# Kernel tuning notes

Measured on AMD Instinct MI355X. Metric: run time of the kernel, lower is better.

Reference implementation:

```python
import jax, jax.numpy as jnp
import numpy as np

DIM = 1024
N_HEADS = 16
N_KV_HEADS = 4
HEAD_DIM = 64
BATCH = 1
SEQ = 4096
ROPE_BASE = 1000.0


def _rope_tables(seq_len, head_dim, base):
    theta = 1.0 / base ** (jnp.arange(0, head_dim, 2, dtype=jnp.float32) / head_dim)
    freqs = jnp.outer(jnp.arange(seq_len, dtype=jnp.float32), theta)  # [S, hd/2]
    return jnp.cos(freqs), jnp.sin(freqs)


def _apply_rope(x, cos, sin):
    # x: [B, S, H, hd]; cos/sin: [S, hd/2] -> broadcast [1, S, 1, hd/2]
    c = cos[None, :, None, :]
    s = sin[None, :, None, :]
    x1, x2 = x[..., ::2], x[..., 1::2]
    even = x1 * c - x2 * s
    odd = x1 * s + x2 * c
    return jnp.stack([even, odd], axis=-1).reshape(x.shape)


def setup_inputs() -> dict:
    key = jax.random.key(0)
    kx, kq, kk, kv, ko = jax.random.split(key, 5)
    x = jax.random.normal(kx, (BATCH, SEQ, DIM), dtype=jnp.float32)
    # causal mask (1 = attend, 0 = masked)
    mask = jnp.tril(jnp.ones((SEQ, SEQ), dtype=jnp.int32))[None, None, :, :]
    scale = DIM ** -0.5
    Wq = jax.random.normal(kq, (DIM, N_HEADS * HEAD_DIM), dtype=jnp.float32) * scale
    Wk = jax.random.normal(kk, (DIM, N_KV_HEADS * HEAD_DIM), dtype=jnp.float32) * scale
    Wv = jax.random.normal(kv, (DIM, N_KV_HEADS * HEAD_DIM), dtype=jnp.float32) * scale
    Wo = jax.random.normal(ko, (N_HEADS * HEAD_DIM, DIM), dtype=jnp.float32) * scale
    return {"x": x, "mask": mask, "Wq": Wq, "Wk": Wk, "Wv": Wv, "Wo": Wo}


def reference(x, mask, Wq, Wk, Wv, Wo):
    batch, seq_len, _ = x.shape
    q = (x @ Wq).reshape(batch, seq_len, N_HEADS, HEAD_DIM)
    k = (x @ Wk).reshape(batch, seq_len, N_KV_HEADS, HEAD_DIM)
    v = (x @ Wv).reshape(batch, seq_len, N_KV_HEADS, HEAD_DIM)
    cos, sin = _rope_tables(seq_len, HEAD_DIM, ROPE_BASE)
    q = _apply_rope(q, cos, sin)
    k = _apply_rope(k, cos, sin)
    rep = N_HEADS // N_KV_HEADS
    k = jnp.repeat(k, rep, axis=2)  # [B, S, H, hd]
    v = jnp.repeat(v, rep, axis=2)
    q = q.transpose(0, 2, 1, 3)  # [B, H, S, hd]
    k = k.transpose(0, 2, 1, 3)
    v = v.transpose(0, 2, 1, 3)
    scale = HEAD_DIM ** -0.5
    scores = jnp.einsum('bhqd,bhkd->bhqk', q, k) * scale  # [B, H, S, S]
    scores = jnp.where(mask == 0, -jnp.inf, scores)
    attn = jax.nn.softmax(scores, axis=-1)
    out = jnp.einsum('bhqk,bhkd->bhqd', attn, v)
    out = out.transpose(0, 2, 1, 3).reshape(batch, seq_len, N_HEADS * HEAD_DIM)
    return out @ Wo
```

## Files before the change

### kernel.cpp

```cpp
#include <hip/hip_runtime.h>
#include <hip/hip_bf16.h>

typedef __attribute__((ext_vector_type(8))) short short8;
typedef __attribute__((ext_vector_type(4))) float f32x4;
typedef unsigned short u16;
typedef unsigned int u32;

#define SEQ 4096

__device__ __forceinline__ u16 f2bf(float f) {
  return __builtin_bit_cast(u16, __float2bfloat16(f));
}

#if __has_builtin(__builtin_amdgcn_exp2f)
#define EXP2(x) __builtin_amdgcn_exp2f(x)
#else
#define EXP2(x) exp2f(x)
#endif

__device__ __forceinline__ u32 pk2(float a, float b) {
  u32 ua = __builtin_bit_cast(u32, a) + 0x8000u;
  u32 ub = __builtin_bit_cast(u32, b) + 0x8000u;
  return __builtin_amdgcn_perm(ub, ua, 0x07060302);
}

__device__ __forceinline__ u32 pk2t(float a, float b) {
  return __builtin_amdgcn_perm(__builtin_bit_cast(u32, b),
                               __builtin_bit_cast(u32, a), 0x07060302);
}

typedef __attribute__((address_space(1))) u32 gas_u32;
typedef __attribute__((address_space(3))) u32 las_u32;
__device__ __forceinline__ void gload16(const u16* g, const u16* l) {
  __builtin_amdgcn_global_load_lds((gas_u32*)(unsigned long long)(const void*)g,
                                   (las_u32*)(u32)(unsigned long long)(const void*)l,
                                   16, 0, 0);
}

#define VM_DRAIN() asm volatile("s_waitcnt vmcnt(0)" ::: "memory")

__global__ __launch_bounds__(256) void k_prep(const float* __restrict__ x,
                                              u16* __restrict__ xb,
                                              float* __restrict__ cosT,
                                              float* __restrict__ sinT) {
  int bid = blockIdx.x;
  if (bid < 4096) {
    int i = bid * 256 + threadIdx.x;
    float4 v = ((const float4*)x)[i];
    u32 lo = (u32)f2bf(v.x) | ((u32)f2bf(v.y) << 16);
    u32 hi = (u32)f2bf(v.z) | ((u32)f2bf(v.w) << 16);
    uint2 o; o.x = lo; o.y = hi;
    ((uint2*)xb)[i] = o;
  } else {
    int tid = (bid - 4096) * 256 + threadIdx.x;
    int pos = tid >> 5, j = tid & 31;
    float theta = exp2f(-0.311430758895f * (float)j);
    float a = (float)pos * theta;
    float s, c;
    sincosf(a, &s, &c);
    cosT[tid] = c;
    sinT[tid] = s;
  }
}

__global__ __launch_bounds__(256) void k_tconvW(const float* __restrict__ Wq,
                                                const float* __restrict__ Wk,
                                                const float* __restrict__ Wv,
                                                const float* __restrict__ Wo,
                                                u16* __restrict__ Wt,
                                                u16* __restrict__ Wto) {
  __shared__ float tile[64][65];
  int bid = blockIdx.x;
  const float* src; u16* dst; int sstride, bx, by;
  if (bid < 256)      { src = Wq; dst = Wt;              sstride = 1024; bx = bid & 15;        by = bid >> 4; }
  else if (bid < 320) { src = Wk; dst = Wt + 1024 * 1024; sstride = 256;  bx = (bid - 256) & 3; by = (bid - 256) >> 2; }
  else if (bid < 384) { src = Wv; dst = Wt + 1280 * 1024; sstride = 256;  bx = (bid - 320) & 3; by = (bid - 320) >> 2; }
  else                { src = Wo; dst = Wto;             sstride = 1024; bx = (bid - 384) & 15; by = (bid - 384) >> 4; }
  const int dstride = 1024;
  int br = by * 64, bc = bx * 64;
  int t = threadIdx.x;
#pragma unroll
  for (int i = 0; i < 16; ++i) {
    int idx = t + i * 256;
    int r = idx >> 6, c = idx & 63;
    tile[r][c] = src[(long)(br + r) * sstride + bc + c];
  }
  __syncthreads();
#pragma unroll
  for (int i = 0; i < 16; ++i) {
    int idx = t + i * 256;
    int cc = idx >> 6, rr = idx & 63;
    dst[(long)(bc + cc) * dstride + br + rr] = f2bf(tile[rr][cc]);
  }
}

__global__ __launch_bounds__(256) void k_gemm(const u16* __restrict__ A,
                                              const u16* __restrict__ Bt,
                                              float* __restrict__ C,
                                              int M, int N, int K) {
  __shared__ __align__(16) u16 a_lds[128 * 64];
  __shared__ __align__(16) u16 b_lds[64 * 64];
  const int bm = blockIdx.x * 128, bn = blockIdx.y * 64;
  const int t = threadIdx.x;
  const int l = t & 63, w = t >> 6;
  const int wm = (w >> 1) * 64, wn = (w & 1) * 32;
  const int lg = l >> 4, ll = l & 15;

  const f32x4 vzero = {0.f, 0.f, 0.f, 0.f};
  f32x4 acc[4][2];
#pragma unroll
  for (int i = 0; i < 4; ++i)
#pragma unroll
    for (int j = 0; j < 2; ++j) acc[i][j] = vzero;

  const u16* ga = A + (long)(bm + w * 32 + (l >> 3)) * K + (l & 7) * 8;
  const u16* gb = Bt + (long)(bn + w * 16 + (l >> 3)) * K + (l & 7) * 8;
  u16* la = a_lds + w * 32 * 64;
  u16* lb = b_lds + w * 16 * 64;
  const long rstep = (long)8 * K;

  for (int kt = 0; kt < K; kt += 64) {
    __syncthreads();
#pragma unroll
    for (int i = 0; i < 4; ++i) gload16(ga + i * rstep, la + i * 512);
#pragma unroll
    for (int i = 0; i < 2; ++i) gload16(gb + i * rstep, lb + i * 512);
    ga += 64; gb += 64;
    __syncthreads();
#pragma unroll
    for (int kc = 0; kc < 2; ++kc) {
      short8 af[4], bfr[2];
#pragma unroll
      for (int mi = 0; mi < 4; ++mi)
        af[mi] = *(const short8*)(a_lds + (wm + mi * 16 + ll) * 64 + kc * 32 + lg * 8);
#pragma unroll
      for (int nb = 0; nb < 2; ++nb)
        bfr[nb] = *(const short8*)(b_lds + (wn + nb * 16 + ll) * 64 + kc * 32 + lg * 8);
#pragma unroll
      for (int mi = 0; mi < 4; ++mi)
#pragma unroll
        for (int nb = 0; nb < 2; ++nb)
          acc[mi][nb] = __builtin_amdgcn_mfma_f32_16x16x32_bf16(af[mi], bfr[nb],
                                                                acc[mi][nb], 0, 0, 0);
    }
  }
  const int rbase = bm + wm + lg * 4;
  const int cbase = bn + wn + ll;
#pragma unroll
  for (int mi = 0; mi < 4; ++mi)
#pragma unroll
    for (int nb = 0; nb < 2; ++nb)
#pragma unroll
      for (int r = 0; r < 4; ++r)
        C[(long)(rbase + mi * 16 + r) * N + cbase + nb * 16] = acc[mi][nb][r];
}

__global__ __launch_bounds__(256) void k_gemmqkv(const u16* __restrict__ A,
                                                 const u16* __restrict__ Bt,
                                                 const float* __restrict__ cosT,
                                                 const float* __restrict__ sinT,
                                                 u16* __restrict__ qb,
                                                 u16* __restrict__ kb,
                                                 u16* __restrict__ vb) {
  const int K = 1024;
  __shared__ __align__(16) u16 a_lds[128 * 64];
  __shared__ __align__(16) u16 b_lds[64 * 64];
  const int bm = blockIdx.x * 128, bn = blockIdx.y * 64;
  const int t = threadIdx.x;
  const int l = t & 63, w = t >> 6;
  const int wm = (w >> 1) * 64, wn = (w & 1) * 32;
  const int lg = l >> 4, ll = l & 15;

  const f32x4 vzero = {0.f, 0.f, 0.f, 0.f};
  f32x4 acc[4][2];
#pragma unroll
  for (int i = 0; i < 4; ++i)
#pragma unroll
    for (int j = 0; j < 2; ++j) acc[i][j] = vzero;

  const u16* ga = A + (long)(bm + w * 32 + (l >> 3)) * K + (l & 7) * 8;
  const u16* gb = Bt + (long)(bn + w * 16 + (l >> 3)) * K + (l & 7) * 8;
  u16* la = a_lds + w * 32 * 64;
  u16* lb = b_lds + w * 16 * 64;
  const long rstep = (long)8 * K;

  for (int kt = 0; kt < K; kt += 64) {
    __syncthreads();
#pragma unroll
    for (int i = 0; i < 4; ++i) gload16(ga + i * rstep, la + i * 512);
#pragma unroll
    for (int i = 0; i < 2; ++i) gload16(gb + i * rstep, lb + i * 512);
    ga += 64; gb += 64;
    __syncthreads();
#pragma unroll
    for (int kc = 0; kc < 2; ++kc) {
      short8 af[4], bfr[2];
#pragma unroll
      for (int mi = 0; mi < 4; ++mi)
        af[mi] = *(const short8*)(a_lds + (wm + mi * 16 + ll) * 64 + kc * 32 + lg * 8);
#pragma unroll
      for (int nb = 0; nb < 2; ++nb)
        bfr[nb] = *(const short8*)(b_lds + (wn + nb * 16 + ll) * 64 + kc * 32 + lg * 8);
#pragma unroll
      for (int mi = 0; mi < 4; ++mi)
#pragma unroll
        for (int nb = 0; nb < 2; ++nb)
          acc[mi][nb] = __builtin_amdgcn_mfma_f32_16x16x32_bf16(af[mi], bfr[nb],
                                                                acc[mi][nb], 0, 0, 0);
    }
  }

  const int rbase = bm + wm + lg * 4;
  const int cbase = bn + wn + ll;
  const int by = blockIdx.y;

  if (by < 20) {
    const float scale = (by < 16) ? 0.18033688011112042f : 1.0f;
#pragma unroll
    for (int mi = 0; mi < 4; ++mi)
#pragma unroll
      for (int nb = 0; nb < 2; ++nb) {
        int col = cbase + nb * 16;
        int j = (col & 63) >> 1;
        long hb = (by < 16) ? (long)(col >> 6) * SEQ
                            : (long)((col - 1024) >> 6) * SEQ;
        u16* dst0 = ((by < 16) ? qb : kb) + hb * 64 + (col & 63);
#pragma unroll
        for (int r = 0; r < 4; ++r) {
          float v0 = acc[mi][nb][r];
          float vp = __shfl_xor(v0, 1);
          int row = rbase + mi * 16 + r;
          float c = cosT[(row << 5) + j], s = sinT[(row << 5) + j];
          float res = (ll & 1) ? (vp * s + v0 * c) * scale
                               : (v0 * c - vp * s) * scale;
          dst0[(long)row * 64] = f2bf(res);
        }
      }
  } else {
#pragma unroll
    for (int mi = 0; mi < 4; ++mi)
#pragma unroll
      for (int nb = 0; nb < 2; ++nb) {
        int col = cbase + nb * 16;
        int vd = col - 1280;
        int row0 = rbase + mi * 16;
        int T = row0 & ~63;
        int kb64 = row0 & 63;
        int s0 = (kb64 & 32) + ((kb64 & 12) << 1) + ((kb64 & 16) >> 2);
        uint2 gg;
        gg.x = pk2(acc[mi][nb][0], acc[mi][nb][1]);
        gg.y = pk2(acc[mi][nb][2], acc[mi][nb][3]);
        *(uint2*)(vb + (long)vd * SEQ + T + s0) = gg;
      }
  }
}

__global__ __launch_bounds__(256) void k_attn(const u16* __restrict__ q,
                                              const u16* __restrict__ kk,
                                              const u16* __restrict__ vT,
                                              u16* __restrict__ o) {
  const int b = blockIdx.x;
  const int h = b & 15;
  const int qt = 63 - (b >> 4);
  const int hkv = h >> 2;
  __shared__ __align__(16) u16 kbuf[2][64 * 64];
  __shared__ __align__(16) u16 vbuf[2][64 * 64];
  const int t = threadIdx.x, w = t >> 6, l = t & 63;
  const int lg = l >> 4, ll = l & 15;
  const int grow = w * 16 + ll;
  const f32x4 vzero = {0.f, 0.f, 0.f, 0.f};
  const short8 vones = {0x3F80, 0x3F80, 0x3F80, 0x3F80,
                        0x3F80, 0x3F80, 0x3F80, 0x3F80};

  const int lr = l >> 3, lc = l & 7;
  const int cswz = lc ^ (lr & 7);
  const u16* kbase = kk + (long)hkv * SEQ * 64;
  const u16* vbase = vT + (long)hkv * 64 * SEQ;
  const u16* kcur  = kbase + (long)(w * 16 + lr) * 64 + cswz * 8;
  const u16* vcurA = vbase + (long)(w * 16 + lr) * SEQ + cswz * 8;
  const u16* vcurB = vcurA + (long)8 * SEQ;

  const int g0 = (lg ^ (ll & 7)) << 4;
  const int g1 = ((lg ^ (ll & 7)) ^ 4) << 4;
  const int rbyte = ll * 128;

#define ISSUE(BUF)                                                           \
  {                                                                          \
    u16* kld = kbuf[BUF] + w * 1024;                                         \
    u16* vld = vbuf[BUF] + w * 1024;                                         \
    gload16(kcur, kld);          gload16(kcur + 512, kld + 512);             \
    gload16(vcurA, vld);         gload16(vcurB, vld + 512);                  \
    kcur += 4096; vcurA += 64; vcurB += 64;                                  \
  }

  ISSUE(0);
  int buf = 0;

  const int q0 = qt * 64 + w * 16;
  short8 qa0 = *(const short8*)(q + ((long)(h * SEQ + q0 + ll) * 64 + lg * 8));
  short8 qa1 = *(const short8*)(q + ((long)(h * SEQ + q0 + ll) * 64 + 32 + lg * 8));

  f32x4 Oacc[4] = {vzero, vzero, vzero, vzero};
  f32x4 lsum = vzero;

  for (int kt = 0; kt <= qt; ++kt) {
    VM_DRAIN();
    __syncthreads();
    if (kt < qt) { ISSUE(buf ^ 1); }

    const char* kb_ = (const char*)kbuf[buf] + rbyte;
    const char* vb_ = (const char*)vbuf[buf] + rbyte;
    f32x4 S[4];
    __builtin_amdgcn_s_setprio(1);
#pragma unroll
    for (int st = 0; st < 4; ++st) {
      short8 ka0 = *(const short8*)(kb_ + st * 2048 + g0);
      short8 ka1 = *(const short8*)(kb_ + st * 2048 + g1);
      f32x4 z = vzero;
      z = __builtin_amdgcn_mfma_f32_16x16x32_bf16(ka0, qa0, z, 0, 0, 0);
      z = __builtin_amdgcn_mfma_f32_16x16x32_bf16(ka1, qa1, z, 0, 0, 0);
      S[st] = z;
    }
    __builtin_amdgcn_s_setprio(0);

    if (kt == qt) {
#pragma unroll
      for (int st = 0; st < 4; ++st)
#pragma unroll
        for (int r = 0; r < 4; ++r)
          if (st * 16 + lg * 4 + r > grow) S[st][r] = -__builtin_inff();
    }

    float p[4][4];
#pragma unroll
    for (int st = 0; st < 4; ++st) {
      p[st][0] = EXP2(S[st][0]); p[st][1] = EXP2(S[st][1]);
      p[st][2] = EXP2(S[st][2]); p[st][3] = EXP2(S[st][3]);
    }
    uint4 u0, u1;
    u0.x = pk2t(p[0][0], p[0][1]); u0.y = pk2t(p[0][2], p[0][3]);
    u0.z = pk2t(p[1][0], p[1][1]); u0.w = pk2t(p[1][2], p[1][3]);
    u1.x = pk2t(p[2][0], p[2][1]); u1.y = pk2t(p[2][2], p[2][3]);
    u1.z = pk2t(p[3][0], p[3][1]); u1.w = pk2t(p[3][2], p[3][3]);
    short8 pa0 = __builtin_bit_cast(short8, u0);
    short8 pa1 = __builtin_bit_cast(short8, u1);

    __builtin_amdgcn_s_setprio(1);
    lsum = __builtin_amdgcn_mfma_f32_16x16x32_bf16(pa0, vones, lsum, 0, 0, 0);
#pragma unroll
    for (int nb = 0; nb < 4; ++nb) {
      short8 vv0 = *(const short8*)(vb_ + nb * 2048 + g0);
      Oacc[nb] = __builtin_amdgcn_mfma_f32_16x16x32_bf16(pa0, vv0, Oacc[nb], 0, 0, 0);
    }
    lsum = __builtin_amdgcn_mfma_f32_16x16x32_bf16(pa1, vones, lsum, 0, 0, 0);
#pragma unroll
    for (int nb = 0; nb < 4; ++nb) {
      short8 vv1 = *(const short8*)(vb_ + nb * 2048 + g1);
      Oacc[nb] = __builtin_amdgcn_mfma_f32_16x16x32_bf16(pa1, vv1, Oacc[nb], 0, 0, 0);
    }
    __builtin_amdgcn_s_setprio(0);
    buf ^= 1;
  }
#undef ISSUE

  float i0 = 1.f / lsum[0];
  float i1 = 1.f / lsum[1];
  float i2 = 1.f / lsum[2];
  float i3 = 1.f / lsum[3];
#pragma unroll
  for (int nb = 0; nb < 4; ++nb) {
    int col = h * 64 + nb * 16 + ll;
    o[(long)(q0 + lg * 4 + 0) * 1024 + col] = f2bf(Oacc[nb][0] * i0);
    o[(long)(q0 + lg * 4 + 1) * 1024 + col] = f2bf(Oacc[nb][1] * i1);
    o[(long)(q0 + lg * 4 + 2) * 1024 + col] = f2bf(Oacc[nb][2] * i2);
    o[(long)(q0 + lg * 4 + 3) * 1024 + col] = f2bf(Oacc[nb][3] * i3);
  }
}

extern "C" void kernel_launch(void* const* d_in, const int* in_sizes, int n_in,
                              void* d_out, int out_size, void* d_ws, size_t ws_size,
                              hipStream_t stream) {
  const float* x  = (const float*)d_in[0];
  const float* Wq = (const float*)d_in[2];
  const float* Wk = (const float*)d_in[3];
  const float* Wv = (const float*)d_in[4];
  const float* Wo = (const float*)d_in[5];
  float* out = (float*)d_out;

  char* ws = (char*)d_ws;
  u16* xb    = (u16*)(ws + 25165824);
  u16* Wt    = (u16*)(ws + 33554432);
  u16* Wto   = (u16*)(ws + 36700160);
  u16* qb    = (u16*)(ws + 38797312);
  u16* kb    = (u16*)(ws + 47185920);
  u16* vb    = (u16*)(ws + 49283072);
  float* cosT = (float*)(ws + 51380224);
  float* sinT = (float*)(ws + 51904512);

  k_prep<<<4608, 256, 0, stream>>>(x, xb, cosT, sinT);
  k_tconvW<<<640, 256, 0, stream>>>(Wq, Wk, Wv, Wo, Wt, Wto);

  k_gemmqkv<<<dim3(32, 24), 256, 0, stream>>>(xb, Wt, cosT, sinT, qb, kb, vb);

  k_attn<<<1024, 256, 0, stream>>>(qb, kb, vb, xb);

  k_gemm<<<dim3(32, 16), 256, 0, stream>>>(xb, Wto, out, 4096, 1024, 1024);
}
```

Measured before the change: 110.7 us.

## Split attention KV tile across two waves with LDS reduction of partial outputs

The attention kernel now launches 128 threads per block instead of 256. Each wave handles all 64 query rows but only half of each 64-key tile, rather than 16 query rows over the full tile. The two waves' partial O accumulators and row sums are combined through shared memory at the end, and V fragments are loaded once and reused across four query groups. This cuts redundant K/V LDS reads per wave and raises MFMA reuse. The cost is more accumulator registers, an extra reduction pass, and fewer waves per block to hide latency.

```diff
diff --git a/kernel.cpp b/kernel.cpp
--- a/kernel.cpp
+++ b/kernel.cpp
@@ -255,7 +255,7 @@
   }
 }
 
-__global__ __launch_bounds__(256) void k_attn(const u16* __restrict__ q,
+__global__ __launch_bounds__(128) void k_attn(const u16* __restrict__ q,
                                               const u16* __restrict__ kk,
                                               const u16* __restrict__ vT,
                                               u16* __restrict__ o) {
@@ -265,115 +265,145 @@
   const int hkv = h >> 2;
   __shared__ __align__(16) u16 kbuf[2][64 * 64];
   __shared__ __align__(16) u16 vbuf[2][64 * 64];
+  __shared__ float lsm[2][64];
   const int t = threadIdx.x, w = t >> 6, l = t & 63;
   const int lg = l >> 4, ll = l & 15;
-  const int grow = w * 16 + ll;
   const f32x4 vzero = {0.f, 0.f, 0.f, 0.f};
   const short8 vones = {0x3F80, 0x3F80, 0x3F80, 0x3F80,
                         0x3F80, 0x3F80, 0x3F80, 0x3F80};
 
-  const int lr = l >> 3, lc = l & 7;
-  const int cswz = lc ^ (lr & 7);
+  const int r16 = t >> 3, c8 = t & 7;
+  const int cswz = c8 ^ (r16 & 7);
   const u16* kbase = kk + (long)hkv * SEQ * 64;
   const u16* vbase = vT + (long)hkv * 64 * SEQ;
-  const u16* kcur  = kbase + (long)(w * 16 + lr) * 64 + cswz * 8;
-  const u16* vcurA = vbase + (long)(w * 16 + lr) * SEQ + cswz * 8;
-  const u16* vcurB = vcurA + (long)8 * SEQ;
-
+  const u16* kcur = kbase + (long)r16 * 64 + cswz * 8;
+  const u16* vc0 = vbase + (long)r16 * SEQ + cswz * 8;
+  const u16* vc1 = vc0 + (long)16 * SEQ;
+  const u16* vc2 = vc0 + (long)32 * SEQ;
+  const u16* vc3 = vc0 + (long)48 * SEQ;
+  const int ldst = r16 * 64 + c8 * 8;
+
+  const int kwbyte = w * 32 * 128;
+  const int rbyte = ll * 128;
   const int g0 = (lg ^ (ll & 7)) << 4;
   const int g1 = ((lg ^ (ll & 7)) ^ 4) << 4;
-  const int rbyte = ll * 128;
+  const int gv = ((w * 4 + lg) ^ (ll & 7)) << 4;
 
 #define ISSUE(BUF)                                                           \
   {                                                                          \
-    u16* kld = kbuf[BUF] + w * 1024;                                         \
-    u16* vld = vbuf[BUF] + w * 1024;                                         \
-    gload16(kcur, kld);          gload16(kcur + 512, kld + 512);             \
-    gload16(vcurA, vld);         gload16(vcurB, vld + 512);                  \
-    kcur += 4096; vcurA += 64; vcurB += 64;                                  \
+    u16* kld = kbuf[BUF] + ldst;                                             \
+    u16* vld = vbuf[BUF] + ldst;                                             \
+    gload16(kcur, kld);              gload16(kcur + 1024, kld + 1024);       \
+    gload16(kcur + 2048, kld + 2048); gload16(kcur + 3072, kld + 3072);      \
+    gload16(vc0, vld);               gload16(vc1, vld + 1024);               \
+    gload16(vc2, vld + 2048);        gload16(vc3, vld + 3072);               \
+    kcur += 4096; vc0 += 64; vc1 += 64; vc2 += 64; vc3 += 64;                \
   }
 
   ISSUE(0);
   int buf = 0;
 
-  const int q0 = qt * 64 + w * 16;
-  short8 qa0 = *(const short8*)(q + ((long)(h * SEQ + q0 + ll) * 64 + lg * 8));
-  short8 qa1 = *(const short8*)(q + ((long)(h * SEQ + q0 + ll) * 64 + 32 + lg * 8));
-
-  f32x4 Oacc[4] = {vzero, vzero, vzero, vzero};
-  f32x4 lsum = vzero;
+  const int q0 = qt * 64;
+  short8 qa[4][2];
+#pragma unroll
+  for (int g = 0; g < 4; ++g)
+#pragma unroll
+    for (int c = 0; c < 2; ++c)
+      qa[g][c] = *(const short8*)(q + ((long)(h * SEQ + q0 + g * 16 + ll) * 64 +
+                                       c * 32 + lg * 8));
+
+  f32x4 Oacc[4][4];
+#pragma unroll
+  for (int g = 0; g < 4; ++g)
+#pragma unroll
+    for (int nb = 0; nb < 4; ++nb) Oacc[g][nb] = vzero;
+  f32x4 lsum[4] = {vzero, vzero, vzero, vzero};
 
   for (int kt = 0; kt <= qt; ++kt) {
     VM_DRAIN();
     __syncthreads();
     if (kt < qt) { ISSUE(buf ^ 1); }
 
-    const char* kb_ = (const char*)kbuf[buf] + rbyte;
+    const char* kb_ = (const char*)kbuf[buf] + kwbyte + rbyte;
     const char* vb_ = (const char*)vbuf[buf] + rbyte;
-    f32x4 S[4];
+
+    f32x4 S[2][4];
     __builtin_amdgcn_s_setprio(1);
 #pragma unroll
-    for (int st = 0; st < 4; ++st) {
+    for (int st = 0; st < 2; ++st) {
       short8 ka0 = *(const short8*)(kb_ + st * 2048 + g0);
       short8 ka1 = *(const short8*)(kb_ + st * 2048 + g1);
-      f32x4 z = vzero;
-      z = __builtin_amdgcn_mfma_f32_16x16x32_bf16(ka0, qa0, z, 0, 0, 0);
-      z = __builtin_amdgcn_mfma_f32_16x16x32_bf16(ka1, qa1, z, 0, 0, 0);
-      S[st] = z;
+#pragma unroll
+      for (int g = 0; g < 4; ++g) {
+        f32x4 z = __builtin_amdgcn_mfma_f32_16x16x32_bf16(ka0, qa[g][0], vzero, 0, 0, 0);
+        S[st][g] = __builtin_amdgcn_mfma_f32_16x16x32_bf16(ka1, qa[g][1], z, 0, 0, 0);
+      }
     }
     __builtin_amdgcn_s_setprio(0);
 
     if (kt == qt) {
 #pragma unroll
-      for (int st = 0; st < 4; ++st)
-#pragma unroll
-        for (int r = 0; r < 4; ++r)
-          if (st * 16 + lg * 4 + r > grow) S[st][r] = -__builtin_inff();
+      for (int st = 0; st < 2; ++st)
+#pragma unroll
+        for (int g = 0; g < 4; ++g)
+#pragma unroll
+          for (int r = 0; r < 4; ++r)
+            if (w * 32 + st * 16 + lg * 4 + r > g * 16 + ll)
+              S[st][g][r] = -__builtin_inff();
     }
 
-    float p[4][4];
-#pragma unroll
-    for (int st = 0; st < 4; ++st) {
-      p[st][0] = EXP2(S[st][0]); p[st][1] = EXP2(S[st][1]);
-      p[st][2] = EXP2(S[st][2]); p[st][3] = EXP2(S[st][3]);
+    short8 vv[4];
+#pragma unroll
+    for (int nb = 0; nb < 4; ++nb)
+      vv[nb] = *(const short8*)(vb_ + nb * 2048 + gv);
+
+#pragma unroll
+    for (int g = 0; g < 4; ++g) {
+      float p00 = EXP2(S[0][g][0]), p01 = EXP2(S[0][g][1]);
+      float p02 = EXP2(S[0][g][2]), p03 = EXP2(S[0][g][3]);
+      float p10 = EXP2(S[1][g][0]), p11 = EXP2(S[1][g][1]);
+      float p12 = EXP2(S[1][g][2]), p13 = EXP2(S[1][g][3]);
+      uint4 u;
+      u.x = pk2t(p00, p01); u.y = pk2t(p02, p03);
+      u.z = pk2t(p10, p11); u.w = pk2t(p12, p13);
+      short8 pa = __builtin_bit_cast(short8, u);
+      __builtin_amdgcn_s_setprio(1);
+      lsum[g] = __builtin_amdgcn_mfma_f32_16x16x32_bf16(pa, vones, lsum[g], 0, 0, 0);
+      Oacc[g][0] = __builtin_amdgcn_mfma_f32_16x16x32_bf16(pa, vv[0], Oacc[g][0], 0, 0, 0);
+      Oacc[g][1] = __builtin_amdgcn_mfma_f32_16x16x32_bf16(pa, vv[1], Oacc[g][1], 0, 0, 0);
+      Oacc[g][2] = __builtin_amdgcn_mfma_f32_16x16x32_bf16(pa, vv[2], Oacc[g][2], 0, 0, 0);
+      Oacc[g][3] = __builtin_amdgcn_mfma_f32_16x16x32_bf16(pa, vv[3], Oacc[g][3], 0, 0, 0);
+      __builtin_amdgcn_s_setprio(0);
     }
-    uint4 u0, u1;
-    u0.x = pk2t(p[0][0], p[0][1]); u0.y = pk2t(p[0][2], p[0][3]);
-    u0.z = pk2t(p[1][0], p[1][1]); u0.w = pk2t(p[1][2], p[1][3]);
-    u1.x = pk2t(p[2][0], p[2][1]); u1.y = pk2t(p[2][2], p[2][3]);
-    u1.z = pk2t(p[3][0], p[3][1]); u1.w = pk2t(p[3][2], p[3][3]);
-    short8 pa0 = __builtin_bit_cast(short8, u0);
-    short8 pa1 = __builtin_bit_cast(short8, u1);
-
-    __builtin_amdgcn_s_setprio(1);
-    lsum = __builtin_amdgcn_mfma_f32_16x16x32_bf16(pa0, vones, lsum, 0, 0, 0);
-#pragma unroll
-    for (int nb = 0; nb < 4; ++nb) {
-      short8 vv0 = *(const short8*)(vb_ + nb * 2048 + g0);
-      Oacc[nb] = __builtin_amdgcn_mfma_f32_16x16x32_bf16(pa0, vv0, Oacc[nb], 0, 0, 0);
-    }
-    lsum = __builtin_amdgcn_mfma_f32_16x16x32_bf16(pa1, vones, lsum, 0, 0, 0);
-#pragma unroll
-    for (int nb = 0; nb < 4; ++nb) {
-      short8 vv1 = *(const short8*)(vb_ + nb * 2048 + g1);
-      Oacc[nb] = __builtin_amdgcn_mfma_f32_16x16x32_bf16(pa1, vv1, Oacc[nb], 0, 0, 0);
-    }
-    __builtin_amdgcn_s_setprio(0);
     buf ^= 1;
   }
 #undef ISSUE
 
-  float i0 = 1.f / lsum[0];
-  float i1 = 1.f / lsum[1];
-  float i2 = 1.f / lsum[2];
-  float i3 = 1.f / lsum[3];
-#pragma unroll
-  for (int nb = 0; nb < 4; ++nb) {
-    int col = h * 64 + nb * 16 + ll;
-    o[(long)(q0 + lg * 4 + 0) * 1024 + col] = f2bf(Oacc[nb][0] * i0);
-    o[(long)(q0 + lg * 4 + 1) * 1024 + col] = f2bf(Oacc[nb][1] * i1);
-    o[(long)(q0 + lg * 4 + 2) * 1024 + col] = f2bf(Oacc[nb][2] * i2);
-    o[(long)(q0 + lg * 4 + 3) * 1024 + col] = f2bf(Oacc[nb][3] * i3);
+  __syncthreads();
+  float* myO = w ? (float*)vbuf : (float*)kbuf;
+#pragma unroll
+  for (int g = 0; g < 4; ++g)
+#pragma unroll
+    for (int nb = 0; nb < 4; ++nb)
+#pragma unroll
+      for (int r = 0; r < 4; ++r)
+        myO[(g * 16 + lg * 4 + r) * 64 + nb * 16 + ll] = Oacc[g][nb][r];
+  if (ll == 0) {
+#pragma unroll
+    for (int g = 0; g < 4; ++g)
+#pragma unroll
+      for (int r = 0; r < 4; ++r)
+        lsm[w][g * 16 + lg * 4 + r] = lsum[g][r];
+  }
+  __syncthreads();
+  const float* O0 = (const float*)kbuf;
+  const float* O1 = (const float*)vbuf;
+#pragma unroll 4
+  for (int qq = 0; qq < 32; ++qq) {
+    int qr = w * 32 + qq;
+    float v = O0[qr * 64 + l] + O1[qr * 64 + l];
+    float inv = 1.f / (lsm[0][qr] + lsm[1][qr]);
+    o[(long)(q0 + qr) * 1024 + h * 64 + l] = f2bf(v * inv);
   }
 }
 
@@ -402,7 +432,7 @@
 
   k_gemmqkv<<<dim3(32, 24), 256, 0, stream>>>(xb, Wt, cosT, sinT, qb, kb, vb);
 
-  k_attn<<<1024, 256, 0, stream>>>(qb, kb, vb, xb);
+  k_attn<<<1024, 128, 0, stream>>>(qb, kb, vb, xb);
 
   k_gemm<<<dim3(32, 16), 256, 0, stream>>>(xb, Wto, out, 4096, 1024, 1024);
 }
```

Result: slower. 120.3 us (+8.7%).
